# Kernel tuning notes

Measured on AMD Instinct MI355X. Metric: run time of the kernel, lower is better.

The kernel has to match this reference:

```python
import jax, jax.numpy as jnp
import numpy as np

DIM = 512
HEADS = 8
HEAD_DIM = DIM // HEADS
SCALE = HEAD_DIM ** -0.5


def setup_inputs() -> dict:
    key = jax.random.key(0)
    k1, k2, k3, k4, k5 = jax.random.split(key, 5)
    x = jax.random.normal(k1, (2, 4096, DIM), dtype=jnp.float32)
    # qkv Linear: weight [3*dim, dim], bias [3*dim]; proj: [dim, dim], [dim]
    w_qkv = jax.random.normal(k2, (3 * DIM, DIM), dtype=jnp.float32) * (DIM ** -0.5)
    b_qkv = jax.random.normal(k3, (3 * DIM,), dtype=jnp.float32) * 0.02
    w_proj = jax.random.normal(k4, (DIM, DIM), dtype=jnp.float32) * (DIM ** -0.5)
    b_proj = jax.random.normal(k5, (DIM,), dtype=jnp.float32) * 0.02
    return {"x": x, "w_qkv": w_qkv, "b_qkv": b_qkv, "w_proj": w_proj, "b_proj": b_proj}


def reference(x, w_qkv, b_qkv, w_proj, b_proj):
    B, N, C = x.shape
    qkv = x @ w_qkv.T + b_qkv  # [B, N, 3C]
    qkv = qkv.reshape(B, N, 3, HEADS, HEAD_DIM).transpose(2, 0, 3, 1, 4)  # [3,B,H,N,hd]
    q, k, v = qkv[0], qkv[1], qkv[2]
    attn = jnp.einsum('bhnd,bhmd->bhnm', q, k) * SCALE  # explicit NxN matrix
    attn = jax.nn.softmax(attn, axis=-1)
    out = jnp.einsum('bhnm,bhmd->bhnd', attn, v)  # [B,H,N,hd]
    out = out.transpose(0, 2, 1, 3).reshape(B, N, C)
    return out @ w_proj.T + b_proj
```

## Files before the change

kernel.cpp:

```cpp
#include <hip/hip_runtime.h>

typedef __bf16 bf16x8 __attribute__((ext_vector_type(8)));
typedef __bf16 bf16x4 __attribute__((ext_vector_type(4)));
typedef __bf16 bf16x2 __attribute__((ext_vector_type(2)));
typedef float  floatx4 __attribute__((ext_vector_type(4)));
typedef unsigned int uint32;
typedef uint32 uintx4 __attribute__((ext_vector_type(4)));

#define MFMA16(a,b,c) __builtin_amdgcn_mfma_f32_16x16x32_bf16(a,b,c,0,0,0)

constexpr int DIM  = 512;
constexpr int SEQ  = 4096;
constexpr int HD   = 64;
constexpr float QSCALE = 0.1803368801111244f;

static __device__ inline __bf16 f2bf(float f) {
    unsigned int u = __builtin_bit_cast(unsigned int, f);
    u += 0x7fffu + ((u >> 16) & 1u);
    return __builtin_bit_cast(__bf16, (unsigned short)(u >> 16));
}
#if __has_builtin(__builtin_amdgcn_cvt_pk_bf16_f32)
static __device__ inline bf16x2 pk2(float a, float b) {
    return __builtin_amdgcn_cvt_pk_bf16_f32(a, b);
}
#else
static __device__ inline bf16x2 pk2(float a, float b) {
    bf16x2 r; r[0] = f2bf(a); r[1] = f2bf(b); return r;
}
#endif
#if __has_builtin(__builtin_amdgcn_exp2f)
#define EXP2(x) __builtin_amdgcn_exp2f(x)
#else
#define EXP2(x) exp2f(x)
#endif
static __device__ inline bf16x8 cvt8(floatx4 lo, floatx4 hi) {
    uintx4 w;
    w[0] = __builtin_bit_cast(uint32, pk2(lo[0], lo[1]));
    w[1] = __builtin_bit_cast(uint32, pk2(lo[2], lo[3]));
    w[2] = __builtin_bit_cast(uint32, pk2(hi[0], hi[1]));
    w[3] = __builtin_bit_cast(uint32, pk2(hi[2], hi[3]));
    return __builtin_bit_cast(bf16x8, w);
}

static __device__ inline void gload16(const __bf16* g, __bf16* l) {
#if __has_builtin(__builtin_amdgcn_global_load_lds)
    __builtin_amdgcn_global_load_lds(
        (const __attribute__((address_space(1))) unsigned int*)g,
        (__attribute__((address_space(3))) unsigned int*)l, 16, 0, 0);
#else
    *(bf16x8*)(l + (threadIdx.x & 63)*8) = *(const bf16x8*)g;
#endif
}


__global__ __launch_bounds__(256)
void gemm_qkv(const float* __restrict__ X, const float* __restrict__ W,
              const float* __restrict__ bias,
              __bf16* __restrict__ Qb, __bf16* __restrict__ Kb, __bf16* __restrict__ Vb)
{
    __shared__ __bf16 As[2][128*32];
    __shared__ __bf16 Bs[2][128*32];
    const int tid  = threadIdx.x;
    const int lane = tid & 63;
    const int wave = tid >> 6;
    const int quad = lane >> 4;
    const int l16  = lane & 15;
    const int waveM = wave >> 1, waveN = wave & 1;
    const int mBase = blockIdx.x * 128;
    const int nBase = blockIdx.y * 128;
    const int which = nBase >> 9;

    floatx4 zero = {0.f, 0.f, 0.f, 0.f};
    floatx4 acc[4][4];
    for (int i = 0; i < 4; i++)
        for (int j = 0; j < 4; j++) acc[i][j] = zero;

    const int srow = tid >> 2;
    const int scol = (tid & 3) * 8;

    const float* xp0 = X + (size_t)(mBase + srow)      * DIM + scol;
    const float* xp1 = X + (size_t)(mBase + 64 + srow) * DIM + scol;
    const float* wp0 = W + (size_t)(nBase + srow)      * DIM + scol;
    const float* wp1 = W + (size_t)(nBase + 64 + srow) * DIM + scol;

    floatx4 r[8];
    auto LOAD = [&](int k0) {
        r[0] = *(const floatx4*)(xp0 + k0); r[1] = *(const floatx4*)(xp0 + k0 + 4);
        r[2] = *(const floatx4*)(xp1 + k0); r[3] = *(const floatx4*)(xp1 + k0 + 4);
        r[4] = *(const floatx4*)(wp0 + k0); r[5] = *(const floatx4*)(wp0 + k0 + 4);
        r[6] = *(const floatx4*)(wp1 + k0); r[7] = *(const floatx4*)(wp1 + k0 + 4);
    };
    auto STORE = [&](int b) {
        *(bf16x8*)&As[b][srow*32 + scol]      = cvt8(r[0], r[1]);
        *(bf16x8*)&As[b][(64+srow)*32 + scol] = cvt8(r[2], r[3]);
        *(bf16x8*)&Bs[b][srow*32 + scol]      = cvt8(r[4], r[5]);
        *(bf16x8*)&Bs[b][(64+srow)*32 + scol] = cvt8(r[6], r[7]);
    };

    LOAD(0);
    STORE(0);
    __syncthreads();

    for (int it = 0; it < 16; ++it) {
        const int cur = it & 1;
        if (it < 15) LOAD((it + 1) * 32);

        bf16x8 af[4], bfr[4];
        for (int mi = 0; mi < 4; mi++)
            af[mi]  = *(const bf16x8*)&As[cur][(waveM*64 + mi*16 + l16)*32 + quad*8];
        for (int ni = 0; ni < 4; ni++)
            bfr[ni] = *(const bf16x8*)&Bs[cur][(waveN*64 + ni*16 + l16)*32 + quad*8];
        if (which == 2) {
            for (int mi = 0; mi < 4; mi++)
                for (int ni = 0; ni < 4; ni++)
                    acc[mi][ni] = MFMA16(af[mi], bfr[ni], acc[mi][ni]);
        } else {
            for (int mi = 0; mi < 4; mi++)
                for (int ni = 0; ni < 4; ni++)
                    acc[mi][ni] = MFMA16(bfr[ni], af[mi], acc[mi][ni]);
        }
        if (it < 15) STORE(cur ^ 1);
        __syncthreads();
    }

    if (which == 2) {
        for (int ni = 0; ni < 4; ni++) {
            const int n = nBase + waveN*64 + ni*16 + l16;
            const float bv = bias[n];
            const int h = (n >> 6) & 7;
            const int d = n & 63;
            for (int mi = 0; mi < 4; mi++) {
                const int m0 = mBase + waveM*64 + mi*16 + quad*4;
                const int b  = m0 >> 12;
                const int s0 = m0 & 4095;
                const int bh = (b << 3) | h;
                bf16x4 v;
                for (int rr = 0; rr < 4; rr++) v[rr] = f2bf(acc[mi][ni][rr] + bv);
                size_t off = (((((size_t)bh*128 + (s0 >> 5))*4 + (d >> 4))*64)
                              + ((s0 >> 2) & 3)*16 + (d & 15))*8 + ((s0 >> 4) & 1)*4;
                *(bf16x4*)&Vb[off] = v;
            }
        }
    } else {
        __bf16* dst = (which == 0) ? Qb : Kb;
        for (int ni = 0; ni < 4; ni++) {
            const int n0 = nBase + waveN*64 + ni*16 + quad*4;
            const floatx4 b4 = *(const floatx4*)&bias[n0];
            const int dfull = n0 & 511;
            const int h  = dfull >> 6;
            const int d0 = dfull & 63;
            const int lgrp = ((d0 >> 3) & 3)*16 + l16;
            const int half = d0 >> 5;
            const int slot = d0 & 7;
            for (int mi = 0; mi < 4; mi++) {
                const int m = mBase + waveM*64 + mi*16 + l16;
                const int b = m >> 12, s = m & 4095;
                const int bh = (b << 3) | h;
                bf16x4 v;
                for (int rr = 0; rr < 4; rr++) {
                    float val = acc[mi][ni][rr] + b4[rr];
                    if (which == 0) val *= QSCALE;
                    v[rr] = f2bf(val);
                }
                size_t off = ((((size_t)bh*256 + (s >> 4))*2 + half)*64 + lgrp)*8 + slot;
                *(bf16x4*)&dst[off] = v;
            }
        }
    }
}

__global__ __launch_bounds__(256, 2)
void attn_kernel(const __bf16* __restrict__ Qb, const __bf16* __restrict__ Kb,
                 const __bf16* __restrict__ Vb, __bf16* __restrict__ Ao)
{
    __shared__ __bf16 Ob[3][64*68];
    __shared__ float  Lb[4][64];
    const int tid  = threadIdx.x;
    const int lane = tid & 63;
    const int wave = tid >> 6;
    const int quad = lane >> 4;
    const int l16  = lane & 15;
    const int bh    = blockIdx.x;
    const int qBase = blockIdx.y * 64;

    const __bf16* qg = Qb + (size_t)bh*256*2*512;
    const __bf16* kg = Kb + (size_t)bh*256*2*512;
    const __bf16* vg = Vb + (size_t)bh*128*4*512;

    bf16x8 qf[4][2];
    for (int t = 0; t < 4; t++)
        for (int hb = 0; hb < 2; hb++)
            qf[t][hb] = *(const bf16x8*)(qg
                + ((size_t)((qBase >> 4) + t)*2 + hb)*512 + lane*8);

    floatx4 zero = {0.f, 0.f, 0.f, 0.f};
    floatx4 oacc[4][4];
    for (int t = 0; t < 4; t++)
        for (int od = 0; od < 4; od++) oacc[t][od] = zero;
    floatx4 Lt[4];
    for (int t = 0; t < 4; t++) Lt[t] = zero;

    bf16x8 ones;
    for (int j = 0; j < 8; j++) ones[j] = f2bf(1.0f);

    const int kvBase = wave * 32;

    auto LOADKV = [&](int cc, bf16x8 (&kb)[4], bf16x8 (&vb)[4]) {
        const __bf16* kp = kg + (size_t)(kvBase + cc)*2048 + lane*8;
        const __bf16* vp = vg + (size_t)(kvBase + cc)*2048 + lane*8;
        kb[0] = *(const bf16x8*)(kp);
        kb[1] = *(const bf16x8*)(kp + 512);
        kb[2] = *(const bf16x8*)(kp + 1024);
        kb[3] = *(const bf16x8*)(kp + 1536);
        vb[0] = *(const bf16x8*)(vp);
        vb[1] = *(const bf16x8*)(vp + 512);
        vb[2] = *(const bf16x8*)(vp + 1024);
        vb[3] = *(const bf16x8*)(vp + 1536);
    };
    auto COMPUTE = [&](bf16x8 (&kb)[4], bf16x8 (&vb)[4]) {
        for (int t = 0; t < 4; t++) {
            floatx4 z0 = zero, z1 = zero;
            __builtin_amdgcn_s_setprio(1);
            z0 = MFMA16(kb[0], qf[t][0], z0);
            z0 = MFMA16(kb[1], qf[t][1], z0);
            z1 = MFMA16(kb[2], qf[t][0], z1);
            z1 = MFMA16(kb[3], qf[t][1], z1);
            __builtin_amdgcn_s_setprio(0);
            float e0[4], e1[4];
            for (int rr = 0; rr < 4; rr++) { e0[rr] = EXP2(z0[rr]); e1[rr] = EXP2(z1[rr]); }
            uintx4 w;
            w[0] = __builtin_bit_cast(uint32, pk2(e0[0], e0[1]));
            w[1] = __builtin_bit_cast(uint32, pk2(e0[2], e0[3]));
            w[2] = __builtin_bit_cast(uint32, pk2(e1[0], e1[1]));
            w[3] = __builtin_bit_cast(uint32, pk2(e1[2], e1[3]));
            bf16x8 pb = __builtin_bit_cast(bf16x8, w);
            __builtin_amdgcn_s_setprio(1);
            Lt[t] = MFMA16(ones, pb, Lt[t]);
            oacc[t][0] = MFMA16(vb[0], pb, oacc[t][0]);
            oacc[t][1] = MFMA16(vb[1], pb, oacc[t][1]);
            oacc[t][2] = MFMA16(vb[2], pb, oacc[t][2]);
            oacc[t][3] = MFMA16(vb[3], pb, oacc[t][3]);
            __builtin_amdgcn_s_setprio(0);
        }
    };

    bf16x8 ka[4], va[4], kb2[4], vb2[4];
    LOADKV(0, ka, va);
    for (int c = 0; c < 32; c += 2) {
        LOADKV(c + 1, kb2, vb2);
        COMPUTE(ka, va);
        if (c + 2 < 32) LOADKV(c + 2, ka, va);
        COMPUTE(kb2, vb2);
    }

    if (lane < 16)
        for (int t = 0; t < 4; t++) Lb[wave][t*16 + lane] = Lt[t][0];
    __syncthreads();
    float inv[4];
    for (int t = 0; t < 4; t++) {
        const int q = t*16 + l16;
        inv[t] = 1.0f / (Lb[0][q] + Lb[1][q] + Lb[2][q] + Lb[3][q]);
    }
    if (wave != 0) {
        for (int t = 0; t < 4; t++)
            for (int od = 0; od < 4; od++) {
                bf16x4 v;
                for (int rr = 0; rr < 4; rr++) v[rr] = f2bf(oacc[t][od][rr] * inv[t]);
                *(bf16x4*)&Ob[wave-1][(t*16 + l16)*68 + od*16 + quad*4] = v;
            }
    }
    __syncthreads();
    if (wave == 0) {
        const int b = bh >> 3, h = bh & 7;
        for (int t = 0; t < 4; t++) {
            const int s = qBase + t*16 + l16;
            for (int od = 0; od < 4; od++) {
                bf16x4 o0 = *(const bf16x4*)&Ob[0][(t*16 + l16)*68 + od*16 + quad*4];
                bf16x4 o1 = *(const bf16x4*)&Ob[1][(t*16 + l16)*68 + od*16 + quad*4];
                bf16x4 o2 = *(const bf16x4*)&Ob[2][(t*16 + l16)*68 + od*16 + quad*4];
                bf16x4 v;
                for (int rr = 0; rr < 4; rr++) {
                    float o = oacc[t][od][rr] * inv[t] +
                              (float)o0[rr] + (float)o1[rr] + (float)o2[rr];
                    v[rr] = f2bf(o);
                }
                *(bf16x4*)&Ao[((size_t)(b*SEQ + s))*DIM + h*HD + od*16 + quad*4] = v;
            }
        }
    }
}

__global__ __launch_bounds__(256)
void gemm_proj(const __bf16* __restrict__ A, const float* __restrict__ W,
               const float* __restrict__ bias, float* __restrict__ Out)
{
    __shared__ __bf16 As[2][64*32];
    __shared__ __bf16 Bs[2][64*32];
    const int tid  = threadIdx.x;
    const int lane = tid & 63;
    const int wave = tid >> 6;
    const int quad = lane >> 4;
    const int l16  = lane & 15;
    const int waveM = wave >> 1, waveN = wave & 1;
    const int mBase = blockIdx.x * 64;
    const int nBase = blockIdx.y * 64;

    floatx4 zero = {0.f, 0.f, 0.f, 0.f};
    floatx4 acc[2][2];
    for (int i = 0; i < 2; i++)
        for (int j = 0; j < 2; j++) acc[i][j] = zero;

    const int srow = tid >> 2;
    const int scol = (tid & 3) * 8;

    const __bf16* gA = A + (size_t)(mBase + wave*16 + (lane >> 2))*DIM + (lane & 3)*8;
    const float*  gW = W + (size_t)(nBase + srow)*DIM + scol;

    floatx4 rw0, rw1;
    gload16(gA, &As[0][wave*512]);
    rw0 = *(const floatx4*)(gW);
    rw1 = *(const floatx4*)(gW + 4);
    *(bf16x8*)&Bs[0][srow*32 + scol] = cvt8(rw0, rw1);
    __syncthreads();

    for (int it = 0; it < 16; ++it) {
        const int cur = it & 1;
        if (it < 15) {
            gload16(gA + (it + 1)*32, &As[cur ^ 1][wave*512]);
            rw0 = *(const floatx4*)(gW + (it + 1)*32);
            rw1 = *(const floatx4*)(gW + (it + 1)*32 + 4);
        }
        bf16x8 af[2], bfr[2];
        for (int mi = 0; mi < 2; mi++)
            af[mi]  = *(const bf16x8*)&As[cur][(waveM*32 + mi*16 + l16)*32 + quad*8];
        for (int ni = 0; ni < 2; ni++)
            bfr[ni] = *(const bf16x8*)&Bs[cur][(waveN*32 + ni*16 + l16)*32 + quad*8];
        for (int mi = 0; mi < 2; mi++)
            for (int ni = 0; ni < 2; ni++)
                acc[mi][ni] = MFMA16(af[mi], bfr[ni], acc[mi][ni]);
        if (it < 15)
            *(bf16x8*)&Bs[cur ^ 1][srow*32 + scol] = cvt8(rw0, rw1);
        __syncthreads();
    }

    for (int ni = 0; ni < 2; ni++) {
        const int n = nBase + waveN*32 + ni*16 + l16;
        const float bv = bias[n];
        for (int mi = 0; mi < 2; mi++) {
            const int m0 = mBase + waveM*32 + mi*16 + quad*4;
            for (int rr = 0; rr < 4; rr++)
                Out[(size_t)(m0 + rr)*DIM + n] = acc[mi][ni][rr] + bv;
        }
    }
}

extern "C" void kernel_launch(void* const* d_in, const int* in_sizes, int n_in,
                              void* d_out, int out_size, void* d_ws, size_t ws_size,
                              hipStream_t stream) {
    const float* x      = (const float*)d_in[0];
    const float* w_qkv  = (const float*)d_in[1];
    const float* b_qkv  = (const float*)d_in[2];
    const float* w_proj = (const float*)d_in[3];
    const float* b_proj = (const float*)d_in[4];
    float* out = (float*)d_out;

    __bf16* ws  = (__bf16*)d_ws;
    const size_t PLANE = (size_t)16 * SEQ * HD;
    __bf16* Qbk = ws;
    __bf16* Kbk = ws + PLANE;
    __bf16* Vbk = ws + 2*PLANE;
    __bf16* Aob = ws + 3*PLANE;

    gemm_qkv<<<dim3(64, 12), 256, 0, stream>>>(x, w_qkv, b_qkv, Qbk, Kbk, Vbk);
    attn_kernel<<<dim3(16, 64), 256, 0, stream>>>(Qbk, Kbk, Vbk, Aob);
    gemm_proj<<<dim3(128, 8), 256, 0, stream>>>(Aob, w_proj, b_proj, out);
}
```

Before: 214.5 us.

## Restructure attention to share double-buffered K/V tiles in LDS across waves

Result: slower. 229.7 us (+7.1%).

```diff
diff --git a/kernel.cpp b/kernel.cpp
--- a/kernel.cpp
+++ b/kernel.cpp
@@ -169,123 +169,115 @@
     }
 }
 
-__global__ __launch_bounds__(256, 2)
+__global__ __launch_bounds__(256)
 void attn_kernel(const __bf16* __restrict__ Qb, const __bf16* __restrict__ Kb,
                  const __bf16* __restrict__ Vb, __bf16* __restrict__ Ao)
 {
-    __shared__ __bf16 Ob[3][64*68];
-    __shared__ float  Lb[4][64];
+    __shared__ __bf16 Kl[2][4096];
+    __shared__ __bf16 Vl[2][4096];
     const int tid  = threadIdx.x;
     const int lane = tid & 63;
     const int wave = tid >> 6;
     const int quad = lane >> 4;
     const int l16  = lane & 15;
     const int bh    = blockIdx.x;
-    const int qBase = blockIdx.y * 64;
+    const int qBase = blockIdx.y * 128;
 
     const __bf16* qg = Qb + (size_t)bh*256*2*512;
     const __bf16* kg = Kb + (size_t)bh*256*2*512;
     const __bf16* vg = Vb + (size_t)bh*128*4*512;
 
-    bf16x8 qf[4][2];
-    for (int t = 0; t < 4; t++)
-        for (int hb = 0; hb < 2; hb++)
-            qf[t][hb] = *(const bf16x8*)(qg
-                + ((size_t)((qBase >> 4) + t)*2 + hb)*512 + lane*8);
+    bf16x8 qf[2][2];
+    {
+        const int sgq = (qBase >> 4) + wave*2;
+        for (int t = 0; t < 2; t++)
+            for (int hb = 0; hb < 2; hb++)
+                qf[t][hb] = *(const bf16x8*)(qg + ((size_t)(sgq + t)*2 + hb)*512 + lane*8);
+    }
 
     floatx4 zero = {0.f, 0.f, 0.f, 0.f};
-    floatx4 oacc[4][4];
-    for (int t = 0; t < 4; t++)
+    floatx4 oacc[2][4];
+    for (int t = 0; t < 2; t++)
         for (int od = 0; od < 4; od++) oacc[t][od] = zero;
-    floatx4 Lt[4];
-    for (int t = 0; t < 4; t++) Lt[t] = zero;
+    floatx4 Lt[2];
+    Lt[0] = zero; Lt[1] = zero;
 
     bf16x8 ones;
     for (int j = 0; j < 8; j++) ones[j] = f2bf(1.0f);
 
-    const int kvBase = wave * 32;
-
-    auto LOADKV = [&](int cc, bf16x8 (&kb)[4], bf16x8 (&vb)[4]) {
-        const __bf16* kp = kg + (size_t)(kvBase + cc)*2048 + lane*8;
-        const __bf16* vp = vg + (size_t)(kvBase + cc)*2048 + lane*8;
-        kb[0] = *(const bf16x8*)(kp);
-        kb[1] = *(const bf16x8*)(kp + 512);
-        kb[2] = *(const bf16x8*)(kp + 1024);
-        kb[3] = *(const bf16x8*)(kp + 1536);
-        vb[0] = *(const bf16x8*)(vp);
-        vb[1] = *(const bf16x8*)(vp + 512);
-        vb[2] = *(const bf16x8*)(vp + 1024);
-        vb[3] = *(const bf16x8*)(vp + 1536);
+    auto STAGE = [&](int c, int b) {
+        const __bf16* ks = kg + (size_t)c*4096 + tid*8;
+        const __bf16* vs = vg + (size_t)c*4096 + tid*8;
+        gload16(ks,        &Kl[b][wave*512]);
+        gload16(ks + 2048, &Kl[b][2048 + wave*512]);
+        gload16(vs,        &Vl[b][wave*512]);
+        gload16(vs + 2048, &Vl[b][2048 + wave*512]);
     };
-    auto COMPUTE = [&](bf16x8 (&kb)[4], bf16x8 (&vb)[4]) {
-        for (int t = 0; t < 4; t++) {
-            floatx4 z0 = zero, z1 = zero;
-            __builtin_amdgcn_s_setprio(1);
-            z0 = MFMA16(kb[0], qf[t][0], z0);
-            z0 = MFMA16(kb[1], qf[t][1], z0);
-            z1 = MFMA16(kb[2], qf[t][0], z1);
-            z1 = MFMA16(kb[3], qf[t][1], z1);
-            __builtin_amdgcn_s_setprio(0);
-            float e0[4], e1[4];
-            for (int rr = 0; rr < 4; rr++) { e0[rr] = EXP2(z0[rr]); e1[rr] = EXP2(z1[rr]); }
-            uintx4 w;
-            w[0] = __builtin_bit_cast(uint32, pk2(e0[0], e0[1]));
-            w[1] = __builtin_bit_cast(uint32, pk2(e0[2], e0[3]));
-            w[2] = __builtin_bit_cast(uint32, pk2(e1[0], e1[1]));
-            w[3] = __builtin_bit_cast(uint32, pk2(e1[2], e1[3]));
-            bf16x8 pb = __builtin_bit_cast(bf16x8, w);
-            __builtin_amdgcn_s_setprio(1);
-            Lt[t] = MFMA16(ones, pb, Lt[t]);
-            oacc[t][0] = MFMA16(vb[0], pb, oacc[t][0]);
-            oacc[t][1] = MFMA16(vb[1], pb, oacc[t][1]);
-            oacc[t][2] = MFMA16(vb[2], pb, oacc[t][2]);
-            oacc[t][3] = MFMA16(vb[3], pb, oacc[t][3]);
-            __builtin_amdgcn_s_setprio(0);
-        }
-    };
-
-    bf16x8 ka[4], va[4], kb2[4], vb2[4];
-    LOADKV(0, ka, va);
-    for (int c = 0; c < 32; c += 2) {
-        LOADKV(c + 1, kb2, vb2);
-        COMPUTE(ka, va);
-        if (c + 2 < 32) LOADKV(c + 2, ka, va);
-        COMPUTE(kb2, vb2);
-    }
-
-    if (lane < 16)
-        for (int t = 0; t < 4; t++) Lb[wave][t*16 + lane] = Lt[t][0];
+
+    STAGE(0, 0);
     __syncthreads();
-    float inv[4];
-    for (int t = 0; t < 4; t++) {
-        const int q = t*16 + l16;
-        inv[t] = 1.0f / (Lb[0][q] + Lb[1][q] + Lb[2][q] + Lb[3][q]);
-    }
-    if (wave != 0) {
-        for (int t = 0; t < 4; t++)
-            for (int od = 0; od < 4; od++) {
-                bf16x4 v;
-                for (int rr = 0; rr < 4; rr++) v[rr] = f2bf(oacc[t][od][rr] * inv[t]);
-                *(bf16x4*)&Ob[wave-1][(t*16 + l16)*68 + od*16 + quad*4] = v;
+
+    for (int c = 0; c < 64; ++c) {
+        const int cur = c & 1;
+        if (c < 63) STAGE(c + 1, cur ^ 1);
+
+        bf16x8 kb[4][2], vf[2][4];
+        #pragma unroll
+        for (int j = 0; j < 4; j++)
+            for (int hb = 0; hb < 2; hb++)
+                kb[j][hb] = *(const bf16x8*)&Kl[cur][((j*2 + hb)*64 + lane)*8];
+        #pragma unroll
+        for (int g = 0; g < 2; g++)
+            for (int od = 0; od < 4; od++)
+                vf[g][od] = *(const bf16x8*)&Vl[cur][((g*4 + od)*64 + lane)*8];
+
+        #pragma unroll
+        for (int t = 0; t < 2; t++) {
+            floatx4 z0 = zero, z1 = zero, z2 = zero, z3 = zero;
+            z0 = MFMA16(kb[0][0], qf[t][0], z0); z0 = MFMA16(kb[0][1], qf[t][1], z0);
+            z1 = MFMA16(kb[1][0], qf[t][0], z1); z1 = MFMA16(kb[1][1], qf[t][1], z1);
+            z2 = MFMA16(kb[2][0], qf[t][0], z2); z2 = MFMA16(kb[2][1], qf[t][1], z2);
+            z3 = MFMA16(kb[3][0], qf[t][0], z3); z3 = MFMA16(kb[3][1], qf[t][1], z3);
+            float e0[4], e1[4], e2[4], e3[4];
+            for (int r = 0; r < 4; r++) {
+                e0[r] = EXP2(z0[r]); e1[r] = EXP2(z1[r]);
+                e2[r] = EXP2(z2[r]); e3[r] = EXP2(z3[r]);
             }
-    }
-    __syncthreads();
-    if (wave == 0) {
-        const int b = bh >> 3, h = bh & 7;
-        for (int t = 0; t < 4; t++) {
-            const int s = qBase + t*16 + l16;
-            for (int od = 0; od < 4; od++) {
-                bf16x4 o0 = *(const bf16x4*)&Ob[0][(t*16 + l16)*68 + od*16 + quad*4];
-                bf16x4 o1 = *(const bf16x4*)&Ob[1][(t*16 + l16)*68 + od*16 + quad*4];
-                bf16x4 o2 = *(const bf16x4*)&Ob[2][(t*16 + l16)*68 + od*16 + quad*4];
-                bf16x4 v;
-                for (int rr = 0; rr < 4; rr++) {
-                    float o = oacc[t][od][rr] * inv[t] +
-                              (float)o0[rr] + (float)o1[rr] + (float)o2[rr];
-                    v[rr] = f2bf(o);
-                }
-                *(bf16x4*)&Ao[((size_t)(b*SEQ + s))*DIM + h*HD + od*16 + quad*4] = v;
-            }
+            uintx4 w0, w1;
+            w0[0] = __builtin_bit_cast(uint32, pk2(e0[0], e0[1]));
+            w0[1] = __builtin_bit_cast(uint32, pk2(e0[2], e0[3]));
+            w0[2] = __builtin_bit_cast(uint32, pk2(e1[0], e1[1]));
+            w0[3] = __builtin_bit_cast(uint32, pk2(e1[2], e1[3]));
+            w1[0] = __builtin_bit_cast(uint32, pk2(e2[0], e2[1]));
+            w1[1] = __builtin_bit_cast(uint32, pk2(e2[2], e2[3]));
+            w1[2] = __builtin_bit_cast(uint32, pk2(e3[0], e3[1]));
+            w1[3] = __builtin_bit_cast(uint32, pk2(e3[2], e3[3]));
+            bf16x8 pb0 = __builtin_bit_cast(bf16x8, w0);
+            bf16x8 pb1 = __builtin_bit_cast(bf16x8, w1);
+            Lt[t] = MFMA16(ones, pb0, Lt[t]);
+            Lt[t] = MFMA16(ones, pb1, Lt[t]);
+            oacc[t][0] = MFMA16(vf[0][0], pb0, oacc[t][0]);
+            oacc[t][1] = MFMA16(vf[0][1], pb0, oacc[t][1]);
+            oacc[t][2] = MFMA16(vf[0][2], pb0, oacc[t][2]);
+            oacc[t][3] = MFMA16(vf[0][3], pb0, oacc[t][3]);
+            oacc[t][0] = MFMA16(vf[1][0], pb1, oacc[t][0]);
+            oacc[t][1] = MFMA16(vf[1][1], pb1, oacc[t][1]);
+            oacc[t][2] = MFMA16(vf[1][2], pb1, oacc[t][2]);
+            oacc[t][3] = MFMA16(vf[1][3], pb1, oacc[t][3]);
+        }
+        __syncthreads();
+    }
+
+    float inv[2];
+    inv[0] = 1.0f / Lt[0][0];
+    inv[1] = 1.0f / Lt[1][0];
+    const int b = bh >> 3, h = bh & 7;
+    for (int t = 0; t < 2; t++) {
+        const int s = qBase + wave*32 + t*16 + l16;
+        for (int od = 0; od < 4; od++) {
+            bf16x4 v;
+            for (int rr = 0; rr < 4; rr++) v[rr] = f2bf(oacc[t][od][rr] * inv[t]);
+            *(bf16x4*)&Ao[((size_t)(b*SEQ + s))*DIM + h*HD + od*16 + quad*4] = v;
         }
     }
 }
@@ -372,6 +364,6 @@
     __bf16* Aob = ws + 3*PLANE;
 
     gemm_qkv<<<dim3(64, 12), 256, 0, stream>>>(x, w_qkv, b_qkv, Qbk, Kbk, Vbk);
-    attn_kernel<<<dim3(16, 64), 256, 0, stream>>>(Qbk, Kbk, Vbk, Aob);
+    attn_kernel<<<dim3(16, 32), 256, 0, stream>>>(Qbk, Kbk, Vbk, Aob);
     gemm_proj<<<dim3(128, 8), 256, 0, stream>>>(Aob, w_proj, b_proj, out);
 }
```

## Raise attention occupancy and drop register double-buffered KV prefetch

Applied to the files above, without the earlier changes.

After: 381.9 us. 78.1% more time.

```diff
diff --git a/kernel.cpp b/kernel.cpp
--- a/kernel.cpp
+++ b/kernel.cpp
@@ -169,7 +169,7 @@
     }
 }
 
-__global__ __launch_bounds__(256, 2)
+__global__ __launch_bounds__(256, 4)
 void attn_kernel(const __bf16* __restrict__ Qb, const __bf16* __restrict__ Kb,
                  const __bf16* __restrict__ Vb, __bf16* __restrict__ Ao)
 {
@@ -203,54 +203,42 @@
     bf16x8 ones;
     for (int j = 0; j < 8; j++) ones[j] = f2bf(1.0f);
 
-    const int kvBase = wave * 32;
-
-    auto LOADKV = [&](int cc, bf16x8 (&kb)[4], bf16x8 (&vb)[4]) {
-        const __bf16* kp = kg + (size_t)(kvBase + cc)*2048 + lane*8;
-        const __bf16* vp = vg + (size_t)(kvBase + cc)*2048 + lane*8;
-        kb[0] = *(const bf16x8*)(kp);
-        kb[1] = *(const bf16x8*)(kp + 512);
-        kb[2] = *(const bf16x8*)(kp + 1024);
-        kb[3] = *(const bf16x8*)(kp + 1536);
-        vb[0] = *(const bf16x8*)(vp);
-        vb[1] = *(const bf16x8*)(vp + 512);
-        vb[2] = *(const bf16x8*)(vp + 1024);
-        vb[3] = *(const bf16x8*)(vp + 1536);
-    };
-    auto COMPUTE = [&](bf16x8 (&kb)[4], bf16x8 (&vb)[4]) {
+    const int key_begin = wave * 1024;
+    const __bf16* kptr = kg + (size_t)(key_begin >> 4)*1024 + lane*8;
+    const __bf16* vptr = vg + (size_t)(key_begin >> 5)*2048 + lane*8;
+
+    for (int c = 0; c < 32; ++c) {
+        bf16x8 kb00 = *(const bf16x8*)(kptr);
+        bf16x8 kb01 = *(const bf16x8*)(kptr + 512);
+        bf16x8 kb10 = *(const bf16x8*)(kptr + 1024);
+        bf16x8 kb11 = *(const bf16x8*)(kptr + 1536);
+        bf16x8 vb0  = *(const bf16x8*)(vptr);
+        bf16x8 vb1  = *(const bf16x8*)(vptr + 512);
+        bf16x8 vb2  = *(const bf16x8*)(vptr + 1024);
+        bf16x8 vb3  = *(const bf16x8*)(vptr + 1536);
+        kptr += 2048;
+        vptr += 2048;
+
         for (int t = 0; t < 4; t++) {
             floatx4 z0 = zero, z1 = zero;
-            __builtin_amdgcn_s_setprio(1);
-            z0 = MFMA16(kb[0], qf[t][0], z0);
-            z0 = MFMA16(kb[1], qf[t][1], z0);
-            z1 = MFMA16(kb[2], qf[t][0], z1);
-            z1 = MFMA16(kb[3], qf[t][1], z1);
-            __builtin_amdgcn_s_setprio(0);
+            z0 = MFMA16(kb00, qf[t][0], z0);
+            z0 = MFMA16(kb01, qf[t][1], z0);
+            z1 = MFMA16(kb10, qf[t][0], z1);
+            z1 = MFMA16(kb11, qf[t][1], z1);
             float e0[4], e1[4];
-            for (int rr = 0; rr < 4; rr++) { e0[rr] = EXP2(z0[rr]); e1[rr] = EXP2(z1[rr]); }
+            for (int r = 0; r < 4; r++) { e0[r] = EXP2(z0[r]); e1[r] = EXP2(z1[r]); }
             uintx4 w;
             w[0] = __builtin_bit_cast(uint32, pk2(e0[0], e0[1]));
             w[1] = __builtin_bit_cast(uint32, pk2(e0[2], e0[3]));
             w[2] = __builtin_bit_cast(uint32, pk2(e1[0], e1[1]));
             w[3] = __builtin_bit_cast(uint32, pk2(e1[2], e1[3]));
             bf16x8 pb = __builtin_bit_cast(bf16x8, w);
-            __builtin_amdgcn_s_setprio(1);
             Lt[t] = MFMA16(ones, pb, Lt[t]);
-            oacc[t][0] = MFMA16(vb[0], pb, oacc[t][0]);
-            oacc[t][1] = MFMA16(vb[1], pb, oacc[t][1]);
-            oacc[t][2] = MFMA16(vb[2], pb, oacc[t][2]);
-            oacc[t][3] = MFMA16(vb[3], pb, oacc[t][3]);
-            __builtin_amdgcn_s_setprio(0);
-        }
-    };
-
-    bf16x8 ka[4], va[4], kb2[4], vb2[4];
-    LOADKV(0, ka, va);
-    for (int c = 0; c < 32; c += 2) {
-        LOADKV(c + 1, kb2, vb2);
-        COMPUTE(ka, va);
-        if (c + 2 < 32) LOADKV(c + 2, ka, va);
-        COMPUTE(kb2, vb2);
+            oacc[t][0] = MFMA16(vb0, pb, oacc[t][0]);
+            oacc[t][1] = MFMA16(vb1, pb, oacc[t][1]);
+            oacc[t][2] = MFMA16(vb2, pb, oacc[t][2]);
+            oacc[t][3] = MFMA16(vb3, pb, oacc[t][3]);
+        }
     }
 
     if (lane < 16)
@@ -265,7 +253,7 @@
         for (int t = 0; t < 4; t++)
             for (int od = 0; od < 4; od++) {
                 bf16x4 v;
-                for (int rr = 0; rr < 4; rr++) v[rr] = f2bf(oacc[t][od][rr] * inv[t]);
+                for (int r = 0; r < 4; r++) v[r] = f2bf(oacc[t][od][r] * inv[t]);
                 *(bf16x4*)&Ob[wave-1][(t*16 + l16)*68 + od*16 + quad*4] = v;
             }
     }
@@ -279,10 +267,10 @@
                 bf16x4 o1 = *(const bf16x4*)&Ob[1][(t*16 + l16)*68 + od*16 + quad*4];
                 bf16x4 o2 = *(const bf16x4*)&Ob[2][(t*16 + l16)*68 + od*16 + quad*4];
                 bf16x4 v;
-                for (int rr = 0; rr < 4; rr++) {
-                    float o = oacc[t][od][rr] * inv[t] +
-                              (float)o0[rr] + (float)o1[rr] + (float)o2[rr];
-                    v[rr] = f2bf(o);
+                for (int r = 0; r < 4; r++) {
+                    float o = oacc[t][od][r] * inv[t] +
+                              (float)o0[r] + (float)o1[r] + (float)o2[r];
+                    v[r] = f2bf(o);
                 }
                 *(bf16x4*)&Ao[((size_t)(b*SEQ + s))*DIM + h*HD + od*16 + quad*4] = v;
             }
```
